# Performance work log

Measured on AMD Instinct MI355X. Metric: run time of the kernel, lower is better.

Reference implementation:

```python
import jax, jax.numpy as jnp
import numpy as np

N_NODES = 50000
N_EDGES = 800000
NODE_F = 100     # memory_feats
EDGE_F = 100     # raw edge feature dim
TIME_D = 100     # temporal encoder dimension
HEADS = 2
OUT_F = 100
NEG_SLOPE = 0.2


def setup_inputs() -> dict:
    key = jax.random.key(0)
    ks = jax.random.split(key, 16)
    return {
        'memory': jax.random.normal(ks[0], (N_NODES, NODE_F), jnp.float32),
        'node_ts': jax.random.uniform(ks[1], (N_NODES,), jnp.float32),
        'edge_feats_raw': jax.random.normal(ks[2], (N_EDGES, EDGE_F), jnp.float32),
        'edge_ts': jax.random.uniform(ks[3], (N_EDGES,), jnp.float32),
        'time_w': jax.random.normal(ks[4], (TIME_D,), jnp.float32),
        'time_b': jax.random.normal(ks[5], (TIME_D,), jnp.float32),
        'fc_node_w': jax.random.normal(ks[6], (NODE_F, HEADS * OUT_F), jnp.float32) * 0.1,
        'fc_node_b': jax.random.normal(ks[7], (HEADS * OUT_F,), jnp.float32) * 0.1,
        'fc_edge_w': jax.random.normal(ks[8], (EDGE_F + TIME_D, HEADS * OUT_F), jnp.float32) * 0.1,
        'fc_edge_b': jax.random.normal(ks[9], (HEADS * OUT_F,), jnp.float32) * 0.1,
        'attn_l': jax.random.normal(ks[10], (HEADS, OUT_F), jnp.float32) * 0.1,
        'attn_r': jax.random.normal(ks[11], (HEADS, OUT_F), jnp.float32) * 0.1,
        'attn_e': jax.random.normal(ks[12], (HEADS, OUT_F), jnp.float32) * 0.1,
        'src': jax.random.randint(ks[13], (N_EDGES,), 0, N_NODES, jnp.int32),
        'dst': jax.random.randint(ks[14], (N_EDGES,), 0, N_NODES, jnp.int32),
    }


def _forward(memory, node_ts, edge_feats_raw, edge_ts,
             time_w, time_b, fc_node_w, fc_node_b, fc_edge_w, fc_edge_b,
             attn_l, attn_r, attn_e, src, dst):
    n = memory.shape[0]
    # TemporalEdgePreprocess: Fourier time encoding of (edge_ts - ts[src])
    time_diff = edge_ts - node_ts[src]                                  # [E]
    te = jnp.cos(time_diff[:, None] * time_w[None, :] + time_b[None, :])  # [E, T]
    efeat = jnp.concatenate([edge_feats_raw, te], axis=1)               # [E, EDGE_F+T]

    # EdgeGATConv (eval mode: dropouts are identity)
    node_feat = (memory @ fc_node_w + fc_node_b).reshape(n, HEADS, OUT_F)          # [N,H,F]
    edge_feat = (efeat @ fc_edge_w + fc_edge_b).reshape(-1, HEADS, OUT_F)          # [E,H,F]

    el = jnp.einsum('nhf,hf->nh', node_feat, attn_l)   # [N,H]
    er = jnp.einsum('nhf,hf->nh', node_feat, attn_r)   # [N,H]
    ee = jnp.einsum('ehf,hf->eh', edge_feat, attn_e)   # [E,H]

    el_prime = el[src] + ee                             # u_add_e  [E,H]
    e = el_prime + er[dst]                              # e_add_v  [E,H]
    e = jnp.where(e > 0, e, NEG_SLOPE * e)              # leaky_relu

    # edge_softmax: softmax over incoming edges per destination node, per head
    emax = jax.ops.segment_max(e, dst, num_segments=n)  # [N,H]
    emax = jnp.where(jnp.isfinite(emax), emax, 0.0)     # zero-in-degree safety
    e_exp = jnp.exp(e - emax[dst])                      # [E,H]
    denom = jax.ops.segment_sum(e_exp, dst, num_segments=n)  # [N,H]
    a = e_exp / denom[dst]                              # [E,H]

    # msg_fn: m = a * el_prime (el_prime has singleton feature dim in torch code)
    m = a * el_prime                                    # [E,H]
    ft = jax.ops.segment_sum(m, dst, num_segments=n)    # [N,H]  (== [N,H,1] features)

    # residual: Identity since memory_feats == out_feats -> view(N,-1,F) = [N,1,F]
    rst = ft[:, :, None] + memory[:, None, :]           # [N,H,F] via broadcast
    return rst.mean(axis=1)                             # .mean(1) over heads -> [N,F]


def reference(memory, node_ts, edge_feats_raw, edge_ts,
              time_w, time_b, fc_node_w, fc_node_b, fc_edge_w, fc_edge_b,
              attn_l, attn_r, attn_e, src, dst):
    return _forward(memory, node_ts, edge_feats_raw, edge_ts,
                    time_w, time_b, fc_node_w, fc_node_b, fc_edge_w, fc_edge_b,
                    attn_l, attn_r, attn_e, src, dst)
```

## Files before the change

### kernel.cpp

```cpp
#include <hip/hip_runtime.h>


constexpr int F = 100;
constexpr float NEG_SLOPE = 0.2f;
constexpr int EPB = 32;

__device__ __forceinline__ float wave_reduce(float v) {
#pragma unroll
    for (int off = 32; off > 0; off >>= 1)
        v += __shfl_down(v, off, 64);
    return v;
}

__global__ void precompute_kernel(
    const float* __restrict__ fc_node_w, const float* __restrict__ fc_node_b,
    const float* __restrict__ fc_edge_w, const float* __restrict__ fc_edge_b,
    const float* __restrict__ attn_l, const float* __restrict__ attn_r,
    const float* __restrict__ attn_e,
    float4* __restrict__ w_node, float2* __restrict__ w_edge,
    float* __restrict__ bias)
{
    int wid  = blockIdx.x * (blockDim.x >> 6) + (threadIdx.x >> 6);
    int lane = threadIdx.x & 63;
    if (wid < F) {
        int t = wid;
        float a0 = 0.f, a1 = 0.f, a2 = 0.f, a3 = 0.f;
        for (int f = lane; f < F; f += 64) {
            float w0 = fc_node_w[t * 2 * F + f];
            float w1 = fc_node_w[t * 2 * F + F + f];
            a0 += w0 * attn_l[f];
            a1 += w1 * attn_l[F + f];
            a2 += w0 * attn_r[f];
            a3 += w1 * attn_r[F + f];
        }
        a0 = wave_reduce(a0); a1 = wave_reduce(a1);
        a2 = wave_reduce(a2); a3 = wave_reduce(a3);
        if (lane == 0) w_node[t] = make_float4(a0, a1, a2, a3);
    } else if (wid < 3 * F) {
        int t = wid - F;
        float a0 = 0.f, a1 = 0.f;
        for (int f = lane; f < F; f += 64) {
            a0 += fc_edge_w[t * 2 * F + f] * attn_e[f];
            a1 += fc_edge_w[t * 2 * F + F + f] * attn_e[F + f];
        }
        a0 = wave_reduce(a0); a1 = wave_reduce(a1);
        if (lane == 0) w_edge[t] = make_float2(a0, a1);
    } else if (wid < 3 * F + 6) {
        int j = wid - 3 * F;
        const float* b  = (j < 4) ? fc_node_b : fc_edge_b;
        const float* av = (j < 2) ? attn_l : (j < 4 ? attn_r : attn_e);
        int h = j & 1;
        float a0 = 0.f;
        for (int f = lane; f < F; f += 64)
            a0 += b[h * F + f] * av[h * F + f];
        a0 = wave_reduce(a0);
        if (lane == 0) bias[j] = a0;
    }
}

__global__ void node_kernel(const float* __restrict__ memory,
                            const float4* __restrict__ w_node,
                            const float* __restrict__ bias,
                            float4* __restrict__ el_er,
                            float4* __restrict__ node_acc, int N)
{
    int n    = blockIdx.x * (blockDim.x >> 6) + (threadIdx.x >> 6);
    int lane = threadIdx.x & 63;
    if (n >= N) return;
    const float* mrow = memory + (size_t)n * F;
    float a0 = 0.f, a1 = 0.f, a2 = 0.f, a3 = 0.f;
    for (int k = lane; k < F; k += 64) {
        float m  = mrow[k];
        float4 w = w_node[k];
        a0 += m * w.x; a1 += m * w.y; a2 += m * w.z; a3 += m * w.w;
    }
    a0 = wave_reduce(a0); a1 = wave_reduce(a1);
    a2 = wave_reduce(a2); a3 = wave_reduce(a3);
    if (lane == 0) {
        el_er[n]    = make_float4(a0 + bias[0], a1 + bias[1],
                                  a2 + bias[2], a3 + bias[3]);
        node_acc[n] = make_float4(0.f, 0.f, 0.f, 0.f);
    }
}

__global__ void edge_gemv_kernel(
    const float* __restrict__ edge_raw,
    const float* __restrict__ edge_ts,
    const float* __restrict__ node_ts,
    const int* __restrict__ src,
    const int* __restrict__ dst,
    const float* __restrict__ time_w,
    const float* __restrict__ time_b,
    const float2* __restrict__ w_edge,
    const float* __restrict__ bias,
    const float4* __restrict__ el_er,
    float4* __restrict__ edge_y, int E)
{
    __shared__ float  tile[EPB * F];
    __shared__ float4 lw4[F];
    __shared__ float2 lt2[F];
    __shared__ float  td_s[EPB];
    __shared__ float2 el_s[EPB];
    __shared__ float2 er_s[EPB];

    const int  t  = threadIdx.x;
    const long eb = (long)blockIdx.x * EPB;

    const float4* g4 = (const float4*)edge_raw;
    const long base4 = eb * 25;
    const long tot4  = (long)E * 25;
#pragma unroll
    for (int r = 0; r < 4; ++r) {
        int idx = t + r * 256;
        if (idx < EPB * 25 && base4 + idx < tot4)
            ((float4*)tile)[idx] = g4[base4 + idx];
    }
    if (t < F) {
        float2 wr = w_edge[t];
        float2 wt = w_edge[F + t];
        lw4[t] = make_float4(wr.x, wr.y, wt.x, wt.y);
        lt2[t] = make_float2(time_w[t], time_b[t]);
    }
    if (t < EPB) {
        long e = eb + t;
        if (e < E) {
            int s = src[e], d = dst[e];
            td_s[t] = edge_ts[e] - node_ts[s];
            float4 a = el_er[s];
            float4 b = el_er[d];
            el_s[t] = make_float2(a.x, a.y);
            er_s[t] = make_float2(b.z, b.w);
        }
    }
    __syncthreads();

    const int el_ = t >> 3;
    const int s8  = t & 7;
    const float td = td_s[el_];
    float a0 = 0.f, a1 = 0.f;
#pragma unroll
    for (int i = 0; i < 13; ++i) {
        int k = s8 + 8 * i;
        if (k < F) {
            float  r  = tile[el_ * F + k];
            float4 w  = lw4[k];
            float2 tm = lt2[k];
            float  c  = __cosf(fmaf(td, tm.x, tm.y));
            a0 = fmaf(r, w.x, fmaf(c, w.z, a0));
            a1 = fmaf(r, w.y, fmaf(c, w.w, a1));
        }
    }
    a0 += __shfl_down(a0, 4, 64);  a1 += __shfl_down(a1, 4, 64);
    a0 += __shfl_down(a0, 2, 64);  a1 += __shfl_down(a1, 2, 64);
    a0 += __shfl_down(a0, 1, 64);  a1 += __shfl_down(a1, 1, 64);

    if (s8 == 0) {
        long e = eb + el_;
        if (e < E) {
            float elp0 = el_s[el_].x + a0 + bias[4];
            float elp1 = el_s[el_].y + a1 + bias[5];
            float e0 = elp0 + er_s[el_].x;
            float e1 = elp1 + er_s[el_].y;
            e0 = e0 > 0.f ? e0 : NEG_SLOPE * e0;
            e1 = e1 > 0.f ? e1 : NEG_SLOPE * e1;
            float x0 = __expf(e0);
            float x1 = __expf(e1);
            edge_y[e] = make_float4(x0 * elp0, x1 * elp1, x0, x1);
        }
    }
}

__global__ void scatter_kernel(const float4* __restrict__ edge_y,
                               const int* __restrict__ dst,
                               float* __restrict__ node_acc, int E)
{
    int i = blockIdx.x * blockDim.x + threadIdx.x;
    if (i >= E) return;
    float4 y = edge_y[i];
    int d = dst[i];
    float* acc = node_acc + (size_t)d * 4;
    atomicAdd(acc + 0, y.x);
    atomicAdd(acc + 1, y.y);
    atomicAdd(acc + 2, y.z);
    atomicAdd(acc + 3, y.w);
}

__global__ void out_kernel(const float* __restrict__ memory,
                           const float4* __restrict__ node_acc,
                           float* __restrict__ out, int N)
{
    int i = blockIdx.x * blockDim.x + threadIdx.x;
    int total = N * (F / 2);
    if (i >= total) return;
    int n = i / (F / 2);
    float4 acc = node_acc[n];
    float ft0 = (acc.z != 0.f) ? acc.x / acc.z : 0.f;
    float ft1 = (acc.w != 0.f) ? acc.y / acc.w : 0.f;
    float add = 0.5f * (ft0 + ft1);
    float2 m = ((const float2*)memory)[i];
    float2 o;
    o.x = m.x + add;
    o.y = m.y + add;
    ((float2*)out)[i] = o;
}

extern "C" void kernel_launch(void* const* d_in, const int* in_sizes, int n_in,
                              void* d_out, int out_size, void* d_ws, size_t ws_size,
                              hipStream_t stream)
{
    const float* memory     = (const float*)d_in[0];
    const float* node_ts    = (const float*)d_in[1];
    const float* edge_raw   = (const float*)d_in[2];
    const float* edge_ts    = (const float*)d_in[3];
    const float* time_w     = (const float*)d_in[4];
    const float* time_b     = (const float*)d_in[5];
    const float* fc_node_w  = (const float*)d_in[6];
    const float* fc_node_b  = (const float*)d_in[7];
    const float* fc_edge_w  = (const float*)d_in[8];
    const float* fc_edge_b  = (const float*)d_in[9];
    const float* attn_l     = (const float*)d_in[10];
    const float* attn_r     = (const float*)d_in[11];
    const float* attn_e     = (const float*)d_in[12];
    const int*   src        = (const int*)d_in[13];
    const int*   dst        = (const int*)d_in[14];
    float*       out        = (float*)d_out;

    const int N = in_sizes[1];
    const int E = in_sizes[3];

    float* ws = (float*)d_ws;
    float4* w_node   = (float4*)ws;
    float2* w_edge   = (float2*)(ws + 400);
    float*  bias     = ws + 800;
    float4* el_er    = (float4*)(ws + 816);
    float4* node_acc = (float4*)(ws + 816 + 4 * (size_t)N);
    float4* edge_y   = (float4*)(ws + 816 + 8 * (size_t)N);

    {
        int waves  = 3 * F + 6;
        int blocks = (waves + 3) / 4;
        precompute_kernel<<<blocks, 256, 0, stream>>>(
            fc_node_w, fc_node_b, fc_edge_w, fc_edge_b,
            attn_l, attn_r, attn_e, w_node, w_edge, bias);
    }
    {
        int blocks = (N + 3) / 4;
        node_kernel<<<blocks, 256, 0, stream>>>(
            memory, w_node, bias, el_er, node_acc, N);
    }
    {
        int blocks = (E + EPB - 1) / EPB;
        edge_gemv_kernel<<<blocks, 256, 0, stream>>>(
            edge_raw, edge_ts, node_ts, src, dst, time_w, time_b,
            w_edge, bias, el_er, edge_y, E);
    }
    {
        int blocks = (E + 255) / 256;
        scatter_kernel<<<blocks, 256, 0, stream>>>(
            edge_y, dst, (float*)node_acc, E);
    }
    {
        int total  = N * (F / 2);
        int blocks = (total + 255) / 256;
        out_kernel<<<blocks, 256, 0, stream>>>(memory, node_acc, out, N);
    }
}
```

Before: 665.0 us.

## Replicate scatter accumulators and read edge rows directly with float4 weights

The scatter stage now spreads atomics across NREP copies of the node accumulator, chosen by lane, which cuts atomic contention on hot destinations. A new finalize kernel reduces the copies and precomputes the per-node add term, and zeroing moves into a separate kernel. The edge GEMV drops the shared-memory staging of edge rows: each thread loads float4 chunks straight from global memory against weights repacked into float4 shared arrays. The costs are an extra pass over 8x accumulator memory and two more launches, and the direct row loads are strided per thread rather than coalesced.

```diff
diff --git a/kernel.cpp b/kernel.cpp
--- a/kernel.cpp
+++ b/kernel.cpp
@@ -4,6 +4,7 @@
 constexpr int F = 100;
 constexpr float NEG_SLOPE = 0.2f;
 constexpr int EPB = 32;
+constexpr int NREP = 8;
 
 __device__ __forceinline__ float wave_reduce(float v) {
 #pragma unroll
@@ -61,8 +62,7 @@
 __global__ void node_kernel(const float* __restrict__ memory,
                             const float4* __restrict__ w_node,
                             const float* __restrict__ bias,
-                            float4* __restrict__ el_er,
-                            float4* __restrict__ node_acc, int N)
+                            float4* __restrict__ el_er, int N)
 {
     int n    = blockIdx.x * (blockDim.x >> 6) + (threadIdx.x >> 6);
     int lane = threadIdx.x & 63;
@@ -76,11 +76,15 @@
     }
     a0 = wave_reduce(a0); a1 = wave_reduce(a1);
     a2 = wave_reduce(a2); a3 = wave_reduce(a3);
-    if (lane == 0) {
-        el_er[n]    = make_float4(a0 + bias[0], a1 + bias[1],
-                                  a2 + bias[2], a3 + bias[3]);
-        node_acc[n] = make_float4(0.f, 0.f, 0.f, 0.f);
-    }
+    if (lane == 0)
+        el_er[n] = make_float4(a0 + bias[0], a1 + bias[1],
+                               a2 + bias[2], a3 + bias[3]);
+}
+
+__global__ void zero_kernel(float4* __restrict__ acc, int n4)
+{
+    int i = blockIdx.x * blockDim.x + threadIdx.x;
+    if (i < n4) acc[i] = make_float4(0.f, 0.f, 0.f, 0.f);
 }
 
 __global__ void edge_gemv_kernel(
@@ -96,9 +100,7 @@
     const float4* __restrict__ el_er,
     float4* __restrict__ edge_y, int E)
 {
-    __shared__ float  tile[EPB * F];
-    __shared__ float4 lw4[F];
-    __shared__ float2 lt2[F];
+    __shared__ float4 wx4[25], wy4[25], wz4[25], ww4[25], tw4[25], tb4[25];
     __shared__ float  td_s[EPB];
     __shared__ float2 el_s[EPB];
     __shared__ float2 er_s[EPB];
@@ -106,97 +108,121 @@
     const int  t  = threadIdx.x;
     const long eb = (long)blockIdx.x * EPB;
 
-    const float4* g4 = (const float4*)edge_raw;
-    const long base4 = eb * 25;
-    const long tot4  = (long)E * 25;
+    if (t < 25) {
+        float4 x, y, z, w, tw, tb;
 #pragma unroll
-    for (int r = 0; r < 4; ++r) {
-        int idx = t + r * 256;
-        if (idx < EPB * 25 && base4 + idx < tot4)
-            ((float4*)tile)[idx] = g4[base4 + idx];
-    }
-    if (t < F) {
-        float2 wr = w_edge[t];
-        float2 wt = w_edge[F + t];
-        lw4[t] = make_float4(wr.x, wr.y, wt.x, wt.y);
-        lt2[t] = make_float2(time_w[t], time_b[t]);
-    }
-    if (t < EPB) {
-        long e = eb + t;
+        for (int j = 0; j < 4; ++j) {
+            int k = 4 * t + j;
+            float2 wr = w_edge[k];
+            float2 wt = w_edge[F + k];
+            ((float*)&x)[j]  = wr.x;  ((float*)&y)[j]  = wr.y;
+            ((float*)&z)[j]  = wt.x;  ((float*)&w)[j]  = wt.y;
+            ((float*)&tw)[j] = time_w[k];
+            ((float*)&tb)[j] = time_b[k];
+        }
+        wx4[t] = x; wy4[t] = y; wz4[t] = z; ww4[t] = w;
+        tw4[t] = tw; tb4[t] = tb;
+    } else if (t >= 64 && t < 64 + EPB) {
+        int  l = t - 64;
+        long e = eb + l;
         if (e < E) {
             int s = src[e], d = dst[e];
-            td_s[t] = edge_ts[e] - node_ts[s];
+            td_s[l] = edge_ts[e] - node_ts[s];
             float4 a = el_er[s];
             float4 b = el_er[d];
-            el_s[t] = make_float2(a.x, a.y);
-            er_s[t] = make_float2(b.z, b.w);
+            el_s[l] = make_float2(a.x, a.y);
+            er_s[l] = make_float2(b.z, b.w);
         }
     }
     __syncthreads();
 
-    const int el_ = t >> 3;
-    const int s8  = t & 7;
-    const float td = td_s[el_];
+    const int  el_ = t >> 3;
+    const int  s8  = t & 7;
+    const long e   = eb + el_;
     float a0 = 0.f, a1 = 0.f;
+    if (e < E) {
+        const float  td   = td_s[el_];
+        const float4* row = (const float4*)edge_raw + e * 25;
 #pragma unroll
-    for (int i = 0; i < 13; ++i) {
-        int k = s8 + 8 * i;
-        if (k < F) {
-            float  r  = tile[el_ * F + k];
-            float4 w  = lw4[k];
-            float2 tm = lt2[k];
-            float  c  = __cosf(fmaf(td, tm.x, tm.y));
-            a0 = fmaf(r, w.x, fmaf(c, w.z, a0));
-            a1 = fmaf(r, w.y, fmaf(c, w.w, a1));
+        for (int i = 0; i < 4; ++i) {
+            int c = s8 + 8 * i;
+            if (c < 25) {
+                float4 r  = row[c];
+                float4 x  = wx4[c], y = wy4[c], z = wz4[c], w = ww4[c];
+                float4 tw = tw4[c], tb = tb4[c];
+                float c0 = __cosf(fmaf(td, tw.x, tb.x));
+                float c1 = __cosf(fmaf(td, tw.y, tb.y));
+                float c2 = __cosf(fmaf(td, tw.z, tb.z));
+                float c3 = __cosf(fmaf(td, tw.w, tb.w));
+                a0 = fmaf(r.x, x.x, fmaf(c0, z.x, a0));
+                a1 = fmaf(r.x, y.x, fmaf(c0, w.x, a1));
+                a0 = fmaf(r.y, x.y, fmaf(c1, z.y, a0));
+                a1 = fmaf(r.y, y.y, fmaf(c1, w.y, a1));
+                a0 = fmaf(r.z, x.z, fmaf(c2, z.z, a0));
+                a1 = fmaf(r.z, y.z, fmaf(c2, w.z, a1));
+                a0 = fmaf(r.w, x.w, fmaf(c3, z.w, a0));
+                a1 = fmaf(r.w, y.w, fmaf(c3, w.w, a1));
+            }
         }
     }
     a0 += __shfl_down(a0, 4, 64);  a1 += __shfl_down(a1, 4, 64);
     a0 += __shfl_down(a0, 2, 64);  a1 += __shfl_down(a1, 2, 64);
     a0 += __shfl_down(a0, 1, 64);  a1 += __shfl_down(a1, 1, 64);
 
-    if (s8 == 0) {
-        long e = eb + el_;
-        if (e < E) {
-            float elp0 = el_s[el_].x + a0 + bias[4];
-            float elp1 = el_s[el_].y + a1 + bias[5];
-            float e0 = elp0 + er_s[el_].x;
-            float e1 = elp1 + er_s[el_].y;
-            e0 = e0 > 0.f ? e0 : NEG_SLOPE * e0;
-            e1 = e1 > 0.f ? e1 : NEG_SLOPE * e1;
-            float x0 = __expf(e0);
-            float x1 = __expf(e1);
-            edge_y[e] = make_float4(x0 * elp0, x1 * elp1, x0, x1);
-        }
+    if (s8 == 0 && e < E) {
+        float elp0 = el_s[el_].x + a0 + bias[4];
+        float elp1 = el_s[el_].y + a1 + bias[5];
+        float e0 = elp0 + er_s[el_].x;
+        float e1 = elp1 + er_s[el_].y;
+        e0 = e0 > 0.f ? e0 : NEG_SLOPE * e0;
+        e1 = e1 > 0.f ? e1 : NEG_SLOPE * e1;
+        float x0 = __expf(e0);
+        float x1 = __expf(e1);
+        edge_y[e] = make_float4(x0 * elp0, x1 * elp1, x0, x1);
     }
 }
 
 __global__ void scatter_kernel(const float4* __restrict__ edge_y,
                                const int* __restrict__ dst,
-                               float* __restrict__ node_acc, int E)
+                               float* __restrict__ acc, int E, int N)
 {
     int i = blockIdx.x * blockDim.x + threadIdx.x;
     if (i >= E) return;
     float4 y = edge_y[i];
     int d = dst[i];
-    float* acc = node_acc + (size_t)d * 4;
-    atomicAdd(acc + 0, y.x);
-    atomicAdd(acc + 1, y.y);
-    atomicAdd(acc + 2, y.z);
-    atomicAdd(acc + 3, y.w);
+    int r = threadIdx.x & (NREP - 1);
+    float* a = acc + ((size_t)r * N + d) * 4;
+    atomicAdd(a + 0, y.x);
+    atomicAdd(a + 1, y.y);
+    atomicAdd(a + 2, y.z);
+    atomicAdd(a + 3, y.w);
+}
+
+__global__ void finalize_kernel(const float4* __restrict__ acc,
+                                float* __restrict__ addbuf, int N)
+{
+    int n = blockIdx.x * blockDim.x + threadIdx.x;
+    if (n >= N) return;
+    float s0 = 0.f, s1 = 0.f, s2 = 0.f, s3 = 0.f;
+#pragma unroll
+    for (int r = 0; r < NREP; ++r) {
+        float4 v = acc[(size_t)r * N + n];
+        s0 += v.x; s1 += v.y; s2 += v.z; s3 += v.w;
+    }
+    float ft0 = (s2 != 0.f) ? s0 / s2 : 0.f;
+    float ft1 = (s3 != 0.f) ? s1 / s3 : 0.f;
+    addbuf[n] = 0.5f * (ft0 + ft1);
 }
 
 __global__ void out_kernel(const float* __restrict__ memory,
-                           const float4* __restrict__ node_acc,
+                           const float* __restrict__ addbuf,
                            float* __restrict__ out, int N)
 {
     int i = blockIdx.x * blockDim.x + threadIdx.x;
     int total = N * (F / 2);
     if (i >= total) return;
     int n = i / (F / 2);
-    float4 acc = node_acc[n];
-    float ft0 = (acc.z != 0.f) ? acc.x / acc.z : 0.f;
-    float ft1 = (acc.w != 0.f) ? acc.y / acc.w : 0.f;
-    float add = 0.5f * (ft0 + ft1);
+    float add = addbuf[n];
     float2 m = ((const float2*)memory)[i];
     float2 o;
     o.x = m.x + add;
@@ -229,12 +255,13 @@
     const int E = in_sizes[3];
 
     float* ws = (float*)d_ws;
-    float4* w_node   = (float4*)ws;
-    float2* w_edge   = (float2*)(ws + 400);
-    float*  bias     = ws + 800;
-    float4* el_er    = (float4*)(ws + 816);
-    float4* node_acc = (float4*)(ws + 816 + 4 * (size_t)N);
-    float4* edge_y   = (float4*)(ws + 816 + 8 * (size_t)N);
+    float4* w_node  = (float4*)ws;
+    float2* w_edge  = (float2*)(ws + 400);
+    float*  bias    = ws + 800;
+    float4* el_er   = (float4*)(ws + 816);
+    float4* acc     = (float4*)(ws + 816 + 4 * (size_t)N);
+    float*  addbuf  = ws + 816 + 36 * (size_t)N;
+    float4* edge_y  = (float4*)(ws + 816 + 37 * (size_t)N);
 
     {
         int waves  = 3 * F + 6;
@@ -246,7 +273,12 @@
     {
         int blocks = (N + 3) / 4;
         node_kernel<<<blocks, 256, 0, stream>>>(
-            memory, w_node, bias, el_er, node_acc, N);
+            memory, w_node, bias, el_er, N);
+    }
+    {
+        int n4     = NREP * N;
+        int blocks = (n4 + 255) / 256;
+        zero_kernel<<<blocks, 256, 0, stream>>>(acc, n4);
     }
     {
         int blocks = (E + EPB - 1) / EPB;
@@ -257,11 +289,15 @@
     {
         int blocks = (E + 255) / 256;
         scatter_kernel<<<blocks, 256, 0, stream>>>(
-            edge_y, dst, (float*)node_acc, E);
+            edge_y, dst, (float*)acc, E, N);
+    }
+    {
+        int blocks = (N + 255) / 256;
+        finalize_kernel<<<blocks, 256, 0, stream>>>(acc, addbuf, N);
     }
     {
         int total  = N * (F / 2);
         int blocks = (total + 255) / 256;
-        out_kernel<<<blocks, 256, 0, stream>>>(memory, node_acc, out, N);
-    }
-}
+        out_kernel<<<blocks, 256, 0, stream>>>(memory, addbuf, out, N);
+    }
+}
```

New measurement: 650.5 us. 2.2% less time.
